# Performance work log

Measured on AMD Instinct MI355X. Metric: run time of the kernel, lower is better.

Reference implementation:

```python
import jax, jax.numpy as jnp
import numpy as np
import math

EMBED_DIM = 1024
NUM_HEADS = 16
HEAD_DIM = EMBED_DIM // NUM_HEADS
BLOCK_SIZE = 64
NUM_RAND_BLOCKS = 3
B, L = 2, 2048


def _build_sparse_mask(seq_len, block_size, num_rand_blocks, seed=0):
    """BigBird block-sparse mask: global (first/last block) + window (prev/self/next) + random blocks."""
    nb = seq_len // block_size
    bm = np.zeros((nb, nb), dtype=bool)
    # global: first and last blocks attend to all / are attended by all
    bm[0, :] = True
    bm[:, 0] = True
    bm[-1, :] = True
    bm[:, -1] = True
    # sliding window for interior blocks
    for b in range(1, nb - 1):
        bm[b, max(b - 1, 0):b + 2] = True
    # random blocks for interior blocks (deterministic for reproducibility)
    rng = np.random.default_rng(seed)
    for b in range(1, nb - 1):
        avail = [x for x in range(nb) if x != b]
        picks = rng.permutation(len(avail))[:num_rand_blocks]
        for p in picks:
            bm[b, avail[p]] = True
    # expand block mask to token-level [L, L]
    return np.kron(bm, np.ones((block_size, block_size), dtype=bool))


def setup_inputs() -> dict:
    key = jax.random.key(0)
    k0, k1, k2, k3, k4 = jax.random.split(key, 5)
    hidden_states = jax.random.normal(k0, (B, L, EMBED_DIM), dtype=jnp.float32)
    s = 0.02
    # torch nn.Linear weights have shape [out_features, in_features]
    Wq = jax.random.normal(k1, (EMBED_DIM, EMBED_DIM), dtype=jnp.float32) * s
    Wk = jax.random.normal(k2, (EMBED_DIM, EMBED_DIM), dtype=jnp.float32) * s
    Wv = jax.random.normal(k3, (EMBED_DIM, EMBED_DIM), dtype=jnp.float32) * s
    Wo = jax.random.normal(k4, (EMBED_DIM, EMBED_DIM), dtype=jnp.float32) * s
    sparse_mask = jnp.asarray(_build_sparse_mask(L, BLOCK_SIZE, NUM_RAND_BLOCKS))
    return {"hidden_states": hidden_states, "Wq": Wq, "Wk": Wk, "Wv": Wv,
            "Wo": Wo, "sparse_mask": sparse_mask}


def reference(hidden_states, Wq, Wk, Wv, Wo, sparse_mask):
    Bsz, Lq, D = hidden_states.shape
    H, hd = NUM_HEADS, HEAD_DIM
    # projections (Linear no bias): x @ W.T
    q = (hidden_states @ Wq.T).reshape(Bsz, Lq, H, hd).transpose(0, 2, 1, 3)
    k = (hidden_states @ Wk.T).reshape(Bsz, Lq, H, hd).transpose(0, 2, 1, 3)
    v = (hidden_states @ Wv.T).reshape(Bsz, Lq, H, hd).transpose(0, 2, 1, 3)
    # dense scores with block-sparse mask (matches reference module's math)
    scores = jnp.einsum('bhqd,bhkd->bhqk', q, k) / math.sqrt(hd)  # [B,H,L,L]
    scores = jnp.where(sparse_mask[None, None, :, :], scores, -jnp.inf)
    attn = jax.nn.softmax(scores.astype(jnp.float32), axis=-1).astype(scores.dtype)
    out = jnp.einsum('bhqk,bhkd->bhqd', attn, v)
    out = out.transpose(0, 2, 1, 3).reshape(Bsz, Lq, D)
    out = out @ Wo.T
    return out
```

## Files before the change

### kernel.cpp

```cpp
#include <hip/hip_runtime.h>
#include <hip/hip_bf16.h>
#include <stdint.h>

#define LSEQ   2048
#define DMODEL 1024
#define NHEADS 16
#define HDIM   64
#define NB     32
#define BATCH  2
#define NGRP   38
#define NWG_ATTN (32 * NGRP)

typedef unsigned short u16;
typedef __attribute__((ext_vector_type(8))) __bf16 bf16x8;
typedef __attribute__((ext_vector_type(4))) float f32x4;
typedef __attribute__((ext_vector_type(4))) unsigned int u32x4;
typedef __attribute__((ext_vector_type(4))) u16 u16x4;


__device__ __forceinline__ u16 f2b(float f) {
  unsigned b = __float_as_uint(f);
  return (u16)((b + 0x7FFFu + ((b >> 16) & 1u)) >> 16);
}

__device__ __forceinline__ void lds_dma16(const u16* g, u16* l) {
  __builtin_amdgcn_global_load_lds(
      (__attribute__((address_space(1))) const void*)g,
      (__attribute__((address_space(3))) void*)l, 16, 0, 0);
}

__device__ __forceinline__ bool probe_is_bf16(const void* src) {
  const u16* p = (const u16*)src;
  int cnt = 0;
  #pragma unroll
  for (int i = 0; i < 64; ++i) {
    int e = (p[i] >> 7) & 0xFF;
    cnt += (e >= 100 && e <= 140) ? 1 : 0;
  }
  return cnt >= 48;
}

__device__ __forceinline__ bool mask_block(const void* m, int qb, int kb) {
  const unsigned char* p = (const unsigned char*)m;
  size_t e = (size_t)(qb * 64) * LSEQ + (size_t)kb * 64;
  unsigned char b0 = p[0], b1 = p[1], b2 = p[2];
  if (b0 == 1 && b1 == 1) return p[e] != 0;
  if (b0 == 1 && b1 == 0 && b2 == 1) return ((const u16*)m)[e] != 0;
  if (b0 == 1) return ((const unsigned int*)m)[e] != 0;
  if (b0 == 0x80 && b1 == 0x3f) return ((const u16*)m)[e] != 0;
  return ((const float*)m)[e] != 0.0f;
}

__global__ __launch_bounds__(256) void convert_kernel(
    const void* __restrict__ hs, const void* __restrict__ wq,
    const void* __restrict__ wk, const void* __restrict__ wv,
    const void* __restrict__ wo, u16* __restrict__ dst,
    const void* __restrict__ mask, int* __restrict__ skb,
    f32x4* __restrict__ zbuf, int zn4) {
  __shared__ int sflag;
  if (threadIdx.x == 0) sflag = probe_is_bf16(hs) ? 1 : 0;
  __syncthreads();
  bool isbf = sflag != 0;
  if (blockIdx.x == 0 && threadIdx.x < NB) {
    int qb = threadIdx.x;
    int base = (qb == 0) ? 0 : ((qb == 31) ? 32 : (64 + (qb - 1) * 8));
    int cap = (qb == 0 || qb == 31) ? 32 : 8;
    int c = 0;
    for (int kb = 0; kb < NB; ++kb)
      if (mask_block(mask, qb, kb)) skb[base + c++] = kb;
    for (; c < cap; ++c) skb[base + c] = -1;
  }
  const int HS4 = BATCH * LSEQ * DMODEL / 4;
  const int W4 = DMODEL * DMODEL / 4;
  int total4 = HS4 + 4 * W4;
  int stride = gridDim.x * blockDim.x;
  for (int i = blockIdx.x * blockDim.x + threadIdx.x; i < total4; i += stride) {
    const void* src;
    int off;
    if (i < HS4) { src = hs; off = i; }
    else {
      int j = i - HS4;
      int wsel = j >> 18;
      off = j & (W4 - 1);
      src = (wsel == 0) ? wq : (wsel == 1) ? wk : (wsel == 2) ? wv : wo;
    }
    u16x4 v;
    if (isbf) v = ((const u16x4*)src)[off];
    else {
      f32x4 f = ((const f32x4*)src)[off];
      v = (u16x4){f2b(f[0]), f2b(f[1]), f2b(f[2]), f2b(f[3])};
    }
    ((u16x4*)dst)[i] = v;
  }
  for (int i = blockIdx.x * blockDim.x + threadIdx.x; i < zn4; i += stride)
    zbuf[i] = (f32x4){0.f, 0.f, 0.f, 0.f};
}

#define GTM 128
#define GTN 128
#define GBK 32
#define LDSW 32

__global__ __launch_bounds__(256) void gemm_bt(
    const u16* __restrict__ A, const u16* __restrict__ Bw,
    void* __restrict__ C, u16* __restrict__ C2, int M, int N, int K,
    int layout, int is_final, const void* __restrict__ probe_src) {
  __shared__ u16 lA[GTM * LDSW];
  __shared__ u16 lB[GTN * LDSW];
  __shared__ int sflag;
  int t = threadIdx.x;
  int w = t >> 6, l = t & 63, q4 = l >> 4, lc = l & 15;
  int lr = l >> 2, lcc = l & 3;
  int tileM = blockIdx.x * GTM, tileN = blockIdx.y * GTN;
  int wm = (w >> 1) * 64, wn = (w & 1) * 64;
  if (t == 0) sflag = (is_final && !probe_is_bf16(probe_src)) ? 0 : 1;

  f32x4 acc[4][4] = {};

  for (int kt = 0; kt < K; kt += GBK) {
    __syncthreads();
    #pragma unroll
    for (int it = 0; it < 2; ++it) {
      int m = w * 2 + it;
      int row = m * 16 + lr;
      lds_dma16(A + (size_t)(tileM + row) * K + kt + lcc * 8, lA + m * 512);
      lds_dma16(Bw + (size_t)(tileN + row) * K + kt + lcc * 8, lB + m * 512);
    }
    __syncthreads();
    bf16x8 af[4], bf[4];
    #pragma unroll
    for (int i = 0; i < 4; ++i)
      af[i] = *(const bf16x8*)(lA + (wm + i * 16 + lc) * LDSW + q4 * 8);
    #pragma unroll
    for (int j = 0; j < 4; ++j)
      bf[j] = *(const bf16x8*)(lB + (wn + j * 16 + lc) * LDSW + q4 * 8);
    #pragma unroll
    for (int i = 0; i < 4; ++i)
      #pragma unroll
      for (int j = 0; j < 4; ++j)
        acc[i][j] = __builtin_amdgcn_mfma_f32_16x16x32_bf16(af[i], bf[j], acc[i][j], 0, 0, 0);
  }

  bool out_bf = sflag != 0;
  #pragma unroll
  for (int i = 0; i < 4; ++i)
    #pragma unroll
    for (int j = 0; j < 4; ++j) {
      int rowb = tileM + wm + i * 16 + q4 * 4;
      int col = tileN + wn + j * 16 + lc;
      if (layout == 0) {
        #pragma unroll
        for (int r = 0; r < 4; ++r) {
          float v = acc[i][j][r];
          size_t idx = (size_t)(rowb + r) * N + col;
          if (out_bf) ((u16*)C)[idx] = f2b(v);
          else ((float*)C)[idx] = v;
        }
      } else {
        int sel = col >> 10;
        int o = col & 1023;
        int h = o >> 6, d = o & 63;
        int b = rowb >> 11, ll = rowb & 2047;
        if (sel == 2) {
          u16x4 pk = {f2b(acc[i][j][0]), f2b(acc[i][j][1]),
                      f2b(acc[i][j][2]), f2b(acc[i][j][3])};
          *(u16x4*)(C2 + ((size_t)((b * NHEADS + h) * HDIM + d)) * LSEQ + ll) = pk;
        } else {
          float sc = (sel == 0) ? 0.125f : 1.0f;
          #pragma unroll
          for (int r = 0; r < 4; ++r) {
            size_t idx = (size_t)sel * (size_t)(BATCH * NHEADS * LSEQ * HDIM) +
                         (((size_t)(b * NHEADS + h) * LSEQ) + ll + r) * HDIM + d;
            ((u16*)C)[idx] = f2b(acc[i][j][r] * sc);
          }
        }
      }
    }
}

#define LDP 72

__global__ __launch_bounds__(256) void attn_kernel(
    const u16* __restrict__ qb_, const u16* __restrict__ kb_,
    const u16* __restrict__ vt_, const int* __restrict__ skb,
    float* __restrict__ obuf2, float* __restrict__ lbuf2,
    u16* __restrict__ ctx) {
  __shared__ u16 lK[64 * 64];
  __shared__ u16 lV[64 * 64];
  __shared__ u16 lP[4][16 * LDP];
  int i = blockIdx.x;
  int bh = (i & 7) + ((i >> 3) & 3) * 8;
  int g = i >> 5;
  int qb = (g < 4) ? 0 : ((g < 8) ? 31 : (g - 7));
  int t = threadIdx.x, w = t >> 6, l = t & 63, q4 = l >> 4, lc = l & 15;
  int c0 = t, c1 = 256 + t;
  int r0 = c0 >> 3, cc0 = c0 & 7, r1 = c1 >> 3, cc1 = c1 & 7;

  const u16* qp = qb_ + ((size_t)bh * LSEQ + qb * 64 + w * 16 + lc) * HDIM;
  bf16x8 bq0 = *(const bf16x8*)(qp + q4 * 8);
  bf16x8 bq1 = *(const bf16x8*)(qp + 32 + q4 * 8);

  const u16* kp = kb_ + (size_t)bh * LSEQ * HDIM;
  const u16* vp = vt_ + (size_t)bh * HDIM * LSEQ;
  u16* myP = &lP[w][0];

  f32x4 oacc[4];
  #pragma unroll
  for (int d = 0; d < 4; ++d) oacc[d] = (f32x4){0.f, 0.f, 0.f, 0.f};
  float lp = 0.0f;

  for (int it = 0; it < 8; ++it) {
    int kb = skb[g * 8 + it];
    if (kb < 0) break;
    const u16* kblk = kp + (size_t)kb * 64 * HDIM;
    const u16* vblk = vp + kb * 64;
    __syncthreads();
    lds_dma16(kblk + r0 * HDIM + cc0 * 8, lK + w * 512);
    lds_dma16(kblk + r1 * HDIM + cc1 * 8, lK + 2048 + w * 512);
    lds_dma16(vblk + (size_t)r0 * LSEQ + cc0 * 8, lV + w * 512);
    lds_dma16(vblk + (size_t)r1 * LSEQ + cc1 * 8, lV + 2048 + w * 512);
    __syncthreads();

    f32x4 st[4];
    #pragma unroll
    for (int mt = 0; mt < 4; ++mt) {
      bf16x8 k0 = *(const bf16x8*)(lK + (mt * 16 + lc) * 64 + q4 * 8);
      bf16x8 k1 = *(const bf16x8*)(lK + (mt * 16 + lc) * 64 + 32 + q4 * 8);
      f32x4 z = (f32x4){0.f, 0.f, 0.f, 0.f};
      z = __builtin_amdgcn_mfma_f32_16x16x32_bf16(k0, bq0, z, 0, 0, 0);
      z = __builtin_amdgcn_mfma_f32_16x16x32_bf16(k1, bq1, z, 0, 0, 0);
      st[mt] = z;
    }

    #pragma unroll
    for (int mt = 0; mt < 4; ++mt) {
      float p0 = __expf(st[mt][0]), p1 = __expf(st[mt][1]);
      float p2 = __expf(st[mt][2]), p3 = __expf(st[mt][3]);
      lp += (p0 + p1) + (p2 + p3);
      u16x4 pk = {f2b(p0), f2b(p1), f2b(p2), f2b(p3)};
      *(u16x4*)(myP + lc * LDP + mt * 16 + q4 * 4) = pk;
    }

    bf16x8 ap0 = *(const bf16x8*)(myP + lc * LDP + q4 * 8);
    bf16x8 ap1 = *(const bf16x8*)(myP + lc * LDP + 32 + q4 * 8);
    #pragma unroll
    for (int dt = 0; dt < 4; ++dt) {
      bf16x8 v0 = *(const bf16x8*)(lV + (dt * 16 + lc) * 64 + q4 * 8);
      bf16x8 v1 = *(const bf16x8*)(lV + (dt * 16 + lc) * 64 + 32 + q4 * 8);
      oacc[dt] = __builtin_amdgcn_mfma_f32_16x16x32_bf16(ap0, v0, oacc[dt], 0, 0, 0);
      oacc[dt] = __builtin_amdgcn_mfma_f32_16x16x32_bf16(ap1, v1, oacc[dt], 0, 0, 0);
    }
  }

  float ltot = lp;
  ltot += __shfl_xor(ltot, 16);
  ltot += __shfl_xor(ltot, 32);

  if (g >= 8) {
    float inv[4];
    #pragma unroll
    for (int r = 0; r < 4; ++r)
      inv[r] = 1.0f / __shfl(ltot, q4 * 4 + r);
    int b = bh >> 4, h = bh & 15;
    #pragma unroll
    for (int dt = 0; dt < 4; ++dt)
      #pragma unroll
      for (int r = 0; r < 4; ++r) {
        float v = oacc[dt][r] * inv[r];
        int grow = qb * 64 + w * 16 + q4 * 4 + r;
        size_t odx = ((size_t)b * LSEQ + grow) * DMODEL + h * HDIM + dt * 16 + lc;
        ctx[odx] = f2b(v);
      }
  } else {
    int s = (qb == 31) ? 1 : 0;
    if (q4 == 0)
      unsafeAtomicAdd(lbuf2 + ((size_t)bh * 2 + s) * 64 + w * 16 + lc, ltot);
    #pragma unroll
    for (int dt = 0; dt < 4; ++dt)
      #pragma unroll
      for (int r = 0; r < 4; ++r)
        unsafeAtomicAdd(obuf2 + (((size_t)bh * 2 + s) * 64 + w * 16 + q4 * 4 + r) * 64 +
                            dt * 16 + lc, oacc[dt][r]);
  }
}

__global__ __launch_bounds__(256) void normalize2_kernel(
    const float* __restrict__ obuf2, const float* __restrict__ lbuf2,
    u16* __restrict__ ctx) {
  int e4 = blockIdx.x * 256 + threadIdx.x;
  int e = e4 * 4;
  int bh = e >> 13;
  int rem = e & 8191;
  int s = rem >> 12, row = (rem >> 6) & 63, d = rem & 63;
  f32x4 o = *(const f32x4*)(obuf2 + e);
  float linv = 1.0f / lbuf2[(bh * 2 + s) * 64 + row];
  int qb = s ? 31 : 0;
  int b = bh >> 4, h = bh & 15;
  int grow = qb * 64 + row;
  u16x4 pk = {f2b(o[0] * linv), f2b(o[1] * linv), f2b(o[2] * linv), f2b(o[3] * linv)};
  *(u16x4*)(ctx + ((size_t)b * LSEQ + grow) * DMODEL + h * HDIM + d) = pk;
}

extern "C" void kernel_launch(void* const* d_in, const int* in_sizes, int n_in,
                              void* d_out, int out_size, void* d_ws, size_t ws_size,
                              hipStream_t stream) {
  const void* hs = d_in[0];
  const void* wq = d_in[1];
  const void* wk = d_in[2];
  const void* wv = d_in[3];
  const void* wo = d_in[4];
  const void* mask = d_in[5];

  u16* hsb = (u16*)d_ws;
  u16* wqb = hsb + 4 * 1024 * 1024;
  u16* wob = wqb + 3 * 1024 * 1024;
  u16* qbuf = wob + 1024 * 1024;
  u16* kbuf = qbuf + 4 * 1024 * 1024;
  u16* vtb  = kbuf + 4 * 1024 * 1024;
  u16* ctx  = vtb + 4 * 1024 * 1024;
  int* skb  = (int*)(ctx + 4 * 1024 * 1024);
  float* obuf2 = (float*)(skb + 512);
  float* lbuf2 = obuf2 + 32 * 2 * 64 * 64;
  const int ZN4 = (32 * 2 * 64 * 64 + 4096) / 4;

  convert_kernel<<<4096, 256, 0, stream>>>(hs, wq, wk, wv, wo, hsb, mask, skb,
                                           (f32x4*)obuf2, ZN4);

  dim3 gqkv(32, 24);
  gemm_bt<<<gqkv, 256, 0, stream>>>(hsb, wqb, qbuf, vtb, 4096, 3072, 1024, 1, 0, hs);

  attn_kernel<<<NWG_ATTN, 256, 0, stream>>>(qbuf, kbuf, vtb, skb, obuf2, lbuf2, ctx);

  normalize2_kernel<<<256, 256, 0, stream>>>(obuf2, lbuf2, ctx);

  dim3 gout(32, 8);
  gemm_bt<<<gout, 256, 0, stream>>>(ctx, wob, d_out, nullptr, 4096, 1024, 1024, 0, 1, hs);
}
```

Baseline: 211.2 us.

## Load B fragments directly from global and use 64-row tiles for output GEMM

Measured after the change: 231.7 us. 1.1x slower.

```diff
diff --git a/kernel.cpp b/kernel.cpp
--- a/kernel.cpp
+++ b/kernel.cpp
@@ -96,48 +96,50 @@
     zbuf[i] = (f32x4){0.f, 0.f, 0.f, 0.f};
 }
 
-#define GTM 128
-#define GTN 128
 #define GBK 32
-#define LDSW 32
-
+#define TN  128
+
+template <int TM>
 __global__ __launch_bounds__(256) void gemm_bt(
     const u16* __restrict__ A, const u16* __restrict__ Bw,
     void* __restrict__ C, u16* __restrict__ C2, int M, int N, int K,
     int layout, int is_final, const void* __restrict__ probe_src) {
-  __shared__ u16 lA[GTM * LDSW];
-  __shared__ u16 lB[GTN * LDSW];
+  constexpr int NJ = (TM == 128) ? 4 : 2;
+  __shared__ u16 lA[TM * 32];
   __shared__ int sflag;
   int t = threadIdx.x;
   int w = t >> 6, l = t & 63, q4 = l >> 4, lc = l & 15;
   int lr = l >> 2, lcc = l & 3;
-  int tileM = blockIdx.x * GTM, tileN = blockIdx.y * GTN;
-  int wm = (w >> 1) * 64, wn = (w & 1) * 64;
+  int tileM = blockIdx.x * TM, tileN = blockIdx.y * TN;
+  int wm = (TM == 128) ? (w >> 1) * 64 : 0;
+  int wn = (TM == 128) ? (w & 1) * 64 : w * 32;
   if (t == 0) sflag = (is_final && !probe_is_bf16(probe_src)) ? 0 : 1;
 
-  f32x4 acc[4][4] = {};
+  f32x4 acc[4][NJ] = {};
 
   for (int kt = 0; kt < K; kt += GBK) {
+    bf16x8 bf[NJ];
+    #pragma unroll
+    for (int j = 0; j < NJ; ++j)
+      bf[j] = *(const bf16x8*)(Bw + (size_t)(tileN + wn + j * 16 + lc) * K + kt + q4 * 8);
+
     __syncthreads();
     #pragma unroll
-    for (int it = 0; it < 2; ++it) {
-      int m = w * 2 + it;
+    for (int it = 0; it < TM / 64; ++it) {
+      int m = w * (TM / 64) + it;
       int row = m * 16 + lr;
       lds_dma16(A + (size_t)(tileM + row) * K + kt + lcc * 8, lA + m * 512);
-      lds_dma16(Bw + (size_t)(tileN + row) * K + kt + lcc * 8, lB + m * 512);
     }
     __syncthreads();
-    bf16x8 af[4], bf[4];
+
+    bf16x8 af[4];
     #pragma unroll
     for (int i = 0; i < 4; ++i)
-      af[i] = *(const bf16x8*)(lA + (wm + i * 16 + lc) * LDSW + q4 * 8);
-    #pragma unroll
-    for (int j = 0; j < 4; ++j)
-      bf[j] = *(const bf16x8*)(lB + (wn + j * 16 + lc) * LDSW + q4 * 8);
+      af[i] = *(const bf16x8*)(lA + (wm + i * 16 + lc) * 32 + q4 * 8);
     #pragma unroll
     for (int i = 0; i < 4; ++i)
       #pragma unroll
-      for (int j = 0; j < 4; ++j)
+      for (int j = 0; j < NJ; ++j)
         acc[i][j] = __builtin_amdgcn_mfma_f32_16x16x32_bf16(af[i], bf[j], acc[i][j], 0, 0, 0);
   }
 
@@ -145,7 +147,7 @@
   #pragma unroll
   for (int i = 0; i < 4; ++i)
     #pragma unroll
-    for (int j = 0; j < 4; ++j) {
+    for (int j = 0; j < NJ; ++j) {
       int rowb = tileM + wm + i * 16 + q4 * 4;
       int col = tileN + wn + j * 16 + lc;
       if (layout == 0) {
@@ -327,12 +329,12 @@
                                            (f32x4*)obuf2, ZN4);
 
   dim3 gqkv(32, 24);
-  gemm_bt<<<gqkv, 256, 0, stream>>>(hsb, wqb, qbuf, vtb, 4096, 3072, 1024, 1, 0, hs);
+  gemm_bt<128><<<gqkv, 256, 0, stream>>>(hsb, wqb, qbuf, vtb, 4096, 3072, 1024, 1, 0, hs);
 
   attn_kernel<<<NWG_ATTN, 256, 0, stream>>>(qbuf, kbuf, vtb, skb, obuf2, lbuf2, ctx);
 
   normalize2_kernel<<<256, 256, 0, stream>>>(obuf2, lbuf2, ctx);
 
-  dim3 gout(32, 8);
-  gemm_bt<<<gout, 256, 0, stream>>>(ctx, wob, d_out, nullptr, 4096, 1024, 1024, 0, 1, hs);
-}
+  dim3 gout(64, 8);
+  gemm_bt<64><<<gout, 256, 0, stream>>>(ctx, wob, d_out, nullptr, 4096, 1024, 1024, 0, 1, hs);
+}
```
